# Kernel tuning notes

Hardware: AMD Instinct MI355X
Metric: run time of the kernel (lower is better)

## Reference

```python
import jax, jax.numpy as jnp
import numpy as np
from jax.scipy.stats import norm

K = 2               # select_experts
NOISE_EPS = 0.01
LOSS_COEF = 0.01
CV_EPS = 1e-10


def setup_inputs() -> dict:
    key = jax.random.key(0)
    ks = jax.random.split(key, 8)
    N, D, H, E = 8192, 1024, 4096, 8
    s_in = 1.0 / np.sqrt(D)
    s_h = 1.0 / np.sqrt(H)
    return {
        "x": jax.random.normal(ks[0], (N, D), jnp.float32),
        "noise": jax.random.normal(ks[1], (N, E), jnp.float32),
        "w_gate": jax.random.normal(ks[2], (D, E), jnp.float32) * s_in,
        "w_noise": jax.random.normal(ks[3], (D, E), jnp.float32) * s_in,
        "W1": jax.random.normal(ks[4], (E, D, H), jnp.float32) * s_in,
        "b1": jnp.zeros((E, H), jnp.float32),
        "W2": jax.random.normal(ks[5], (E, H, D), jnp.float32) * s_h,
        "b2": jnp.zeros((E, D), jnp.float32),
    }


def _cv_squared(v):
    # torch .var() is unbiased (ddof=1)
    return v.var(ddof=1) / (v.mean() ** 2 + CV_EPS)


def reference(x, noise, w_gate, w_noise, W1, b1, W2, b2):
    N = x.shape[0]
    # --- noisy top-k gating (training path) ---
    clean_logits = x @ w_gate                                  # [N, E]
    noise_stddev = jax.nn.softplus(x @ w_noise) + NOISE_EPS    # [N, E]
    noisy_logits = clean_logits + noise * noise_stddev         # [N, E]
    top_vals, top_idx = jax.lax.top_k(noisy_logits, K + 1)     # [N, K+1]
    top_k_gates = jax.nn.softmax(top_vals[:, :K], axis=1)      # [N, K]
    gates = jnp.zeros_like(noisy_logits).at[
        jnp.arange(N)[:, None], top_idx[:, :K]
    ].set(top_k_gates)                                         # [N, E]

    # --- load (prob of being in top-k under the gating noise) ---
    thr_in = top_vals[:, K:K + 1]                              # [N, 1]
    thr_out = top_vals[:, K - 1:K]                             # [N, 1]
    is_in = noisy_logits > thr_in
    prob_in = norm.cdf((clean_logits - thr_in) / noise_stddev)
    prob_out = norm.cdf((clean_logits - thr_out) / noise_stddev)
    load = jnp.where(is_in, prob_in, prob_out).sum(0)          # [E]

    importance = gates.sum(0)                                  # [E]
    loss = (_cv_squared(importance) + _cv_squared(load)) * LOSS_COEF

    # --- dense all-expert stack, masked by sparse gates ---
    h = jax.nn.relu(jnp.einsum('nd,edh->neh', x, W1) + b1)     # [N, E, H]
    out = jnp.einsum('neh,ehd->ned', h, W2) + b2               # [N, E, D]
    y = jnp.einsum('ned,ne->nd', out, gates)                   # [N, D]
    return y, loss
```

## Files before the change

### kernel.cpp

```cpp
#include <hip/hip_runtime.h>

typedef unsigned short u16;
typedef unsigned int u32;
typedef __attribute__((ext_vector_type(4))) float f32x4;
typedef __attribute__((ext_vector_type(8))) short short8;
typedef __attribute__((ext_vector_type(4))) unsigned short u16x4;

#define BARR __builtin_amdgcn_s_barrier()
#define VM4  asm volatile("s_waitcnt vmcnt(4)" ::: "memory")
#define VM0  asm volatile("s_waitcnt vmcnt(0)" ::: "memory")

__device__ __forceinline__ u16 f2b(float f){
  u32 u = __float_as_uint(f);
  u = (u + 0x7FFFu + ((u >> 16) & 1u)) >> 16;
  return (u16)u;
}
__device__ __forceinline__ float b2f(u16 h){ return __uint_as_float(((u32)h) << 16); }

__device__ __forceinline__ void gload16(const void* g, void* l){
  __builtin_amdgcn_global_load_lds((__attribute__((address_space(1))) void*)(g),
                                   (__attribute__((address_space(3))) void*)(l), 16, 0, 0);
}

__global__ __launch_bounds__(256) void transpose_cvt2_kernel(const float* __restrict__ W1,
                                                             const float* __restrict__ W2,
                                                             u16* __restrict__ w1t,
                                                             u16* __restrict__ w2t){
  __shared__ float t[64][65];
  int z = blockIdx.z;
  const float* src; u16* dst; int R, C, c0, r0; size_t eo;
  if (z < 8){
    src = W1; dst = w1t; R = 1024; C = 4096;
    c0 = blockIdx.x * 64; r0 = blockIdx.y * 64;
    eo = (size_t)R * C * z;
  } else {
    src = W2; dst = w2t; R = 4096; C = 1024;
    c0 = blockIdx.y * 64; r0 = blockIdx.x * 64;
    eo = (size_t)R * C * (z - 8);
  }
  int tid = threadIdx.x;
  int lr = tid >> 4, lc4 = (tid & 15) * 4;
  #pragma unroll
  for (int i = 0; i < 4; i++){
    int r = lr + i * 16;
    float4 v = *(const float4*)&src[eo + (size_t)(r0 + r) * C + c0 + lc4];
    t[r][lc4] = v.x; t[r][lc4 + 1] = v.y; t[r][lc4 + 2] = v.z; t[r][lc4 + 3] = v.w;
  }
  __syncthreads();
  #pragma unroll
  for (int i = 0; i < 4; i++){
    int c = lr + i * 16;
    u16x4 o = { f2b(t[lc4][c]), f2b(t[lc4 + 1][c]), f2b(t[lc4 + 2][c]), f2b(t[lc4 + 3][c]) };
    *(u16x4*)&dst[eo + (size_t)(c0 + c) * R + r0 + lc4] = o;
  }
}

__global__ __launch_bounds__(256) void gating_kernel(const float* __restrict__ x,
                                                     const float* __restrict__ nz,
                                                     const float* __restrict__ wg,
                                                     const float* __restrict__ wn,
                                                     int* __restrict__ counts,
                                                     int4* __restrict__ rowinfo,
                                                     float* __restrict__ loadrow,
                                                     u16* __restrict__ xb){
  __shared__ float wpart[16][4][17];
  int tid = threadIdx.x, w = tid >> 6, lane = tid & 63;
  int d0 = w * 256 + lane * 4;
  float4 wgA[4], wgB[4], wnA[4], wnB[4];
  #pragma unroll
  for (int k = 0; k < 4; k++){
    wgA[k] = *(const float4*)&wg[(d0 + k) * 8];
    wgB[k] = *(const float4*)&wg[(d0 + k) * 8 + 4];
    wnA[k] = *(const float4*)&wn[(d0 + k) * 8];
    wnB[k] = *(const float4*)&wn[(d0 + k) * 8 + 4];
  }
  int rbase = blockIdx.x * 16;
  for (int r = 0; r < 16; r++){
    int row = rbase + r;
    float4 xv = *(const float4*)&x[(size_t)row * 1024 + d0];
    u16x4 xo = { f2b(xv.x), f2b(xv.y), f2b(xv.z), f2b(xv.w) };
    *(u16x4*)&xb[(size_t)row * 1024 + d0] = xo;
    float ag[8], an[8];
    #pragma unroll
    for (int e = 0; e < 8; e++){ ag[e] = 0.f; an[e] = 0.f; }
    float xk[4] = { xv.x, xv.y, xv.z, xv.w };
    #pragma unroll
    for (int k = 0; k < 4; k++){
      ag[0] = fmaf(xk[k], wgA[k].x, ag[0]); ag[1] = fmaf(xk[k], wgA[k].y, ag[1]);
      ag[2] = fmaf(xk[k], wgA[k].z, ag[2]); ag[3] = fmaf(xk[k], wgA[k].w, ag[3]);
      ag[4] = fmaf(xk[k], wgB[k].x, ag[4]); ag[5] = fmaf(xk[k], wgB[k].y, ag[5]);
      ag[6] = fmaf(xk[k], wgB[k].z, ag[6]); ag[7] = fmaf(xk[k], wgB[k].w, ag[7]);
      an[0] = fmaf(xk[k], wnA[k].x, an[0]); an[1] = fmaf(xk[k], wnA[k].y, an[1]);
      an[2] = fmaf(xk[k], wnA[k].z, an[2]); an[3] = fmaf(xk[k], wnA[k].w, an[3]);
      an[4] = fmaf(xk[k], wnB[k].x, an[4]); an[5] = fmaf(xk[k], wnB[k].y, an[5]);
      an[6] = fmaf(xk[k], wnB[k].z, an[6]); an[7] = fmaf(xk[k], wnB[k].w, an[7]);
    }
    #pragma unroll
    for (int off = 32; off >= 1; off >>= 1){
      #pragma unroll
      for (int e = 0; e < 8; e++){
        ag[e] += __shfl_xor(ag[e], off, 64);
        an[e] += __shfl_xor(an[e], off, 64);
      }
    }
    if (lane == 0){
      #pragma unroll
      for (int e = 0; e < 8; e++){
        wpart[r][w][e] = ag[e];
        wpart[r][w][8 + e] = an[e];
      }
    }
  }
  __syncthreads();
  if (tid < 16){
    int r = tid, row = rbase + r;
    float cg[16];
    #pragma unroll
    for (int v = 0; v < 16; v++)
      cg[v] = wpart[r][0][v] + wpart[r][1][v] + wpart[r][2][v] + wpart[r][3][v];
    float clean[8], sd[8], noisy[8];
    #pragma unroll
    for (int e = 0; e < 8; e++){
      clean[e] = cg[e];
      float v = cg[8 + e];
      float sp = fmaxf(v, 0.f) + log1pf(expf(-fabsf(v)));
      sd[e] = sp + 0.01f;
      noisy[e] = clean[e] + nz[row * 8 + e] * sd[e];
    }
    int i0 = 0, i1 = -1;
    float b0 = -3.4e38f, b1v = -3.4e38f, b2v = -3.4e38f;
    #pragma unroll
    for (int j = 0; j < 8; j++){
      float t = noisy[j];
      if (t > b0){ b2v = b1v; b1v = b0; i1 = i0; b0 = t; i0 = j; }
      else if (t > b1v){ b2v = b1v; b1v = t; i1 = j; }
      else if (t > b2v){ b2v = t; }
    }
    float eg = expf(b1v - b0);
    float g0 = 1.f / (1.f + eg), g1 = eg / (1.f + eg);
    rowinfo[row] = make_int4(i0, i1, __float_as_int(g0), __float_as_int(g1));
    atomicAdd(&counts[i0], 1);
    atomicAdd(&counts[i1], 1);
    float thr_in = b2v, thr_out = b1v;
    #pragma unroll
    for (int e = 0; e < 8; e++){
      bool isin = noisy[e] > thr_in;
      float thr = isin ? thr_in : thr_out;
      float z = (clean[e] - thr) / sd[e];
      loadrow[row * 8 + e] = 0.5f * (1.f + erff(z * 0.70710678118654752f));
    }
  }
}

__global__ __launch_bounds__(256) void fill_kernel(const int* __restrict__ counts,
                                                   const int4* __restrict__ rowinfo,
                                                   int* __restrict__ offs,
                                                   int* __restrict__ cnt2,
                                                   int* __restrict__ tok,
                                                   int* __restrict__ slot_of,
                                                   int* __restrict__ btab){
  __shared__ int loff[8];
  if (threadIdx.x == 0){
    int s = 0;
    for (int e = 0; e < 8; e++){ loff[e] = s; s += counts[e]; }
    if (blockIdx.x == 0){
      int nb = 0;
      for (int e = 0; e < 8; e++){
        offs[e] = loff[e];
        int nbe = (counts[e] + 255) >> 8;
        for (int t = 0; t < nbe; t++) btab[nb++] = (e << 16) | t;
      }
      offs[15] = nb;
    }
  }
  __syncthreads();
  int r = blockIdx.x * 256 + threadIdx.x;
  int4 ri = rowinfo[r];
  int p0 = atomicAdd(&cnt2[ri.x], 1);
  int s0 = loff[ri.x] + p0;
  tok[s0] = r; slot_of[2 * r] = s0;
  int p1 = atomicAdd(&cnt2[ri.y], 1);
  int s1 = loff[ri.y] + p1;
  tok[s1] = r; slot_of[2 * r + 1] = s1;
}

template<int KDIM, bool GATHER, bool RELU, bool PSPLIT>
__global__ __launch_bounds__(512, 1) void ffn8_kernel(
    const u16* __restrict__ Ag, const u16* __restrict__ Bt,
    const float* __restrict__ bias, u16* __restrict__ outp,
    const int* __restrict__ counts, const int* __restrict__ offs,
    const int* __restrict__ btab, const int* __restrict__ tok,
    int nc, int klen, int ostr, size_t pstride)
{
  __shared__ u16 As[2][2][128 * 64];
  __shared__ u16 Bs[2][2][128 * 64];

  int gx = gridDim.x;
  int lin = blockIdx.y * gx + blockIdx.x;
  int total = gx * gridDim.y, chunk = total >> 3;
  int swz = (lin & 7) * chunk + (lin >> 3);
  int bx = swz % gx, tq = swz / gx;
  int nblk = offs[15];
  if (bx >= nblk) return;
  int kh = tq / nc;
  int tn = tq - kh * nc;
  int kbase = kh * klen;
  int niter = klen >> 7;
  int et = btab[bx]; int e = et >> 16, tm = et & 0xffff;
  int cnt = counts[e], off_e = offs[e];

  int tid = threadIdx.x, lane = tid & 63;
  int wid = tid >> 6, wm = wid >> 2, wn = wid & 3;

  int rl0 = tid >> 3, c8 = tid & 7;
  const char* Abase = (const char*)Ag + (size_t)kbase * 2;
  const char* Bbase = (const char*)(Bt + (size_t)e * 4194304) + (size_t)kbase * 2;
  u32 aoff[4], boff[4];
  #pragma unroll
  for (int h = 0; h < 2; h++)
    #pragma unroll
    for (int r = 0; r < 2; r++){
      int rl = h * 128 + r * 64 + rl0;
      int c8s = c8 ^ (rl & 7);
      int rr = tm * 256 + rl;
      int rc = (rr < cnt) ? rr : (cnt - 1);
      size_t arow = GATHER ? (size_t)tok[off_e + rc] : (size_t)(off_e + rc);
      aoff[h * 2 + r] = (u32)(arow * (KDIM * 2) + c8s * 16);
      boff[h * 2 + r] = (u32)((size_t)(tn * 256 + rl) * (KDIM * 2) + c8s * 16);
    }
  int ldst = (tid & ~63) * 8;

  auto stA = [&](int b, int h, int t){
    const char* s = Abase + (size_t)t * 128;
    gload16(s + aoff[h * 2 + 0], &As[b][h][ldst]);
    gload16(s + aoff[h * 2 + 1], &As[b][h][4096 + ldst]);
  };
  auto stB = [&](int b, int h, int t){
    const char* s = Bbase + (size_t)t * 128;
    gload16(s + boff[h * 2 + 0], &Bs[b][h][ldst]);
    gload16(s + boff[h * 2 + 1], &Bs[b][h][4096 + ldst]);
  };

  int lm = lane & 15, lkb = (lane >> 4) * 8;
  short8 Ar[4][2], Br[2][2][2];
  auto ldA = [&](int b, int rh){
    #pragma unroll
    for (int ii = 0; ii < 4; ii++){
      int rl = rh * 64 + ii * 16 + lm;
      #pragma unroll
      for (int ks = 0; ks < 2; ks++){
        int idx = (rl * 64 + ks * 32 + lkb) ^ ((rl & 7) << 3);
        Ar[ii][ks] = *(const short8*)&As[b][wm][idx];
      }
    }
  };
  auto ldB = [&](int b, int ch){
    #pragma unroll
    for (int jj = 0; jj < 2; jj++){
      int rb = wn * 64 + ch * 32 + jj * 16 + lm;
      int hB = rb >> 7, rl = rb & 127;
      #pragma unroll
      for (int ks = 0; ks < 2; ks++){
        int idx = (rl * 64 + ks * 32 + lkb) ^ ((rl & 7) << 3);
        Br[ch][jj][ks] = *(const short8*)&Bs[b][hB][idx];
      }
    }
  };

  f32x4 acc[8][4];
  #pragma unroll
  for (int i = 0; i < 8; i++)
    #pragma unroll
    for (int j = 0; j < 4; j++) acc[i][j] = (f32x4){0.f, 0.f, 0.f, 0.f};

  auto mfmaQ = [&](int rh, int ch){
    __builtin_amdgcn_s_setprio(1);
    #pragma unroll
    for (int ks = 0; ks < 2; ks++)
      #pragma unroll
      for (int ii = 0; ii < 4; ii++)
        #pragma unroll
        for (int jj = 0; jj < 2; jj++)
          acc[rh * 4 + ii][ch * 2 + jj] = __builtin_amdgcn_mfma_f32_16x16x32_bf16(
              Ar[ii][ks], Br[ch][jj][ks], acc[rh * 4 + ii][ch * 2 + jj], 0, 0, 0);
    __builtin_amdgcn_s_setprio(0);
  };

  stA(0, 0, 0); stA(0, 1, 0); stB(0, 0, 0); stB(0, 1, 0);
  stB(1, 0, 1); stA(1, 0, 1);
  VM4; BARR;

  for (int j = 0; j < niter - 1; ++j){
    int t1 = 2 * j + 1, t2 = 2 * j + 2, t3 = 2 * j + 3;
    ldA(0, 0); ldB(0, 0);
    stA(1, 1, t1);
    BARR; mfmaQ(0, 0); ldB(0, 1); BARR;
    stB(1, 1, t1);
    BARR; mfmaQ(0, 1); ldA(0, 1); BARR;
    stB(0, 0, t2);
    BARR; mfmaQ(1, 1); BARR;
    stA(0, 0, t2);
    BARR; mfmaQ(1, 0); VM4; BARR;
    ldA(1, 0); ldB(1, 0);
    stA(0, 1, t2);
    BARR; mfmaQ(0, 0); ldB(1, 1); BARR;
    stB(0, 1, t2);
    BARR; mfmaQ(0, 1); ldA(1, 1); BARR;
    stB(1, 0, t3);
    BARR; mfmaQ(1, 1); BARR;
    stA(1, 0, t3);
    BARR; mfmaQ(1, 0); VM4; BARR;
  }

  {
    int t1 = (klen >> 6) - 1;
    ldA(0, 0); ldB(0, 0);
    stA(1, 1, t1);
    BARR; mfmaQ(0, 0); ldB(0, 1); BARR;
    stB(1, 1, t1);
    BARR; mfmaQ(0, 1); ldA(0, 1); BARR;
    BARR; mfmaQ(1, 1); BARR;
    mfmaQ(1, 0); VM0; BARR;
    ldA(1, 0); ldB(1, 0);
    BARR; mfmaQ(0, 0); ldB(1, 1); BARR;
    BARR; mfmaQ(0, 1); ldA(1, 1); BARR;
    BARR; mfmaQ(1, 1); BARR;
    mfmaQ(1, 0);
  }

  int lr = (lane >> 4) * 4;
  u16* po = outp + (PSPLIT ? (size_t)kh * pstride : 0);
  #pragma unroll
  for (int i = 0; i < 8; i++){
    int row_l = wm * 128 + i * 16 + lr;
    #pragma unroll
    for (int jj = 0; jj < 4; jj++){
      int col = tn * 256 + wn * 64 + jj * 16 + lm;
      float bv = PSPLIT ? 0.f : bias[e * ostr + col];
      #pragma unroll
      for (int q = 0; q < 4; q++){
        int r = tm * 256 + row_l + q;
        if (r < cnt){
          float v = acc[i][jj][q] + bv;
          if (RELU) v = fmaxf(v, 0.f);
          po[(size_t)(off_e + r) * ostr + col] = f2b(v);
        }
      }
    }
  }
}

__global__ __launch_bounds__(256) void combine_kernel(const u16* __restrict__ pb,
                                                      const float* __restrict__ b2,
                                                      const int4* __restrict__ rowinfo,
                                                      const int* __restrict__ slot_of,
                                                      float* __restrict__ y){
  const size_t PS = (size_t)16384 * 1024;
  int w = threadIdx.x >> 6, lane = threadIdx.x & 63;
  int row = blockIdx.x * 4 + w;
  int4 ri = rowinfo[row];
  float g0 = __int_as_float(ri.z), g1 = __int_as_float(ri.w);
  int s0 = slot_of[2 * row], s1 = slot_of[2 * row + 1];
  const u16* pa = pb + ((size_t)s0 << 10);
  const u16* pbb = pb + ((size_t)s1 << 10);
  #pragma unroll
  for (int k = 0; k < 4; k++){
    int c4 = k * 256 + lane * 4;
    float4 sum0 = *(const float4*)&b2[(ri.x << 10) + c4];
    float4 sum1 = *(const float4*)&b2[(ri.y << 10) + c4];
    #pragma unroll
    for (int kh = 0; kh < 4; kh++){
      u16x4 a = *(const u16x4*)&pa[kh * PS + c4];
      u16x4 b = *(const u16x4*)&pbb[kh * PS + c4];
      sum0.x += b2f(a.x); sum0.y += b2f(a.y); sum0.z += b2f(a.z); sum0.w += b2f(a.w);
      sum1.x += b2f(b.x); sum1.y += b2f(b.y); sum1.z += b2f(b.z); sum1.w += b2f(b.w);
    }
    float4 o;
    o.x = g0 * sum0.x + g1 * sum1.x;
    o.y = g0 * sum0.y + g1 * sum1.y;
    o.z = g0 * sum0.z + g1 * sum1.z;
    o.w = g0 * sum0.w + g1 * sum1.w;
    *(float4*)&y[(size_t)row * 1024 + c4] = o;
  }
}

__global__ __launch_bounds__(256) void loss1_kernel(const int4* __restrict__ rowinfo,
                                                    const float* __restrict__ loadrow,
                                                    float* __restrict__ partials){
  __shared__ float part[16][256];
  int tid = threadIdx.x;
  int r = blockIdx.x * 256 + tid;
  int4 ri = rowinfo[r];
  float g0 = __int_as_float(ri.z), g1 = __int_as_float(ri.w);
  f32x4 l0 = *(const f32x4*)&loadrow[r * 8];
  f32x4 l1 = *(const f32x4*)&loadrow[r * 8 + 4];
  #pragma unroll
  for (int e = 0; e < 8; e++){
    part[e][tid] = ((ri.x == e) ? g0 : 0.f) + ((ri.y == e) ? g1 : 0.f);
    part[8 + e][tid] = (e < 4) ? l0[e & 3] : l1[e & 3];
  }
  __syncthreads();
  #pragma unroll
  for (int s = 128; s >= 1; s >>= 1){
    if (tid < s){
      #pragma unroll
      for (int e = 0; e < 16; e++) part[e][tid] += part[e][tid + s];
    }
    __syncthreads();
  }
  if (tid < 16) partials[blockIdx.x * 16 + tid] = part[tid][0];
}

__global__ __launch_bounds__(64) void loss2_kernel(const float* __restrict__ partials,
                                                   float* __restrict__ out_loss){
  __shared__ float tot[16];
  int tid = threadIdx.x;
  if (tid < 16){
    float s = 0.f;
    for (int b = 0; b < 32; b++) s += partials[b * 16 + tid];
    tot[tid] = s;
  }
  __syncthreads();
  if (tid == 0){
    float mi = 0.f, ml = 0.f;
    for (int e = 0; e < 8; e++){ mi += tot[e]; ml += tot[8 + e]; }
    mi *= 0.125f; ml *= 0.125f;
    float vi = 0.f, vl = 0.f;
    for (int e = 0; e < 8; e++){
      float di = tot[e] - mi; vi += di * di;
      float dl = tot[8 + e] - ml; vl += dl * dl;
    }
    vi /= 7.f; vl /= 7.f;
    float cvi = vi / (mi * mi + 1e-10f);
    float cvl = vl / (ml * ml + 1e-10f);
    out_loss[0] = 0.01f * (cvi + cvl);
  }
}

extern "C" void kernel_launch(void* const* d_in, const int* in_sizes, int n_in,
                              void* d_out, int out_size, void* d_ws, size_t ws_size,
                              hipStream_t stream){
  const float* x  = (const float*)d_in[0];
  const float* nz = (const float*)d_in[1];
  const float* wg = (const float*)d_in[2];
  const float* wn = (const float*)d_in[3];
  const float* W1 = (const float*)d_in[4];
  const float* b1 = (const float*)d_in[5];
  const float* W2 = (const float*)d_in[6];
  const float* b2 = (const float*)d_in[7];
  float* y = (float*)d_out;
  float* loss = y + (size_t)8192 * 1024;

  char* ws = (char*)d_ws;
  size_t o = 0;
  auto alloc = [&](size_t bytes){ size_t r = o; o += (bytes + 255) & ~(size_t)255; return r; };
  int*  counts  = (int*)(ws + alloc(64));
  int*  cnt2    = (int*)(ws + alloc(64));
  int*  offs    = (int*)(ws + alloc(64));
  int*  btab    = (int*)(ws + alloc(1024));
  int4* rowinfo = (int4*)(ws + alloc((size_t)8192 * 16));
  int*  slot_of = (int*)(ws + alloc((size_t)16384 * 4));
  int*  tok     = (int*)(ws + alloc((size_t)16384 * 4));
  float* loadrow = (float*)(ws + alloc((size_t)8192 * 8 * 4));
  float* partials = (float*)(ws + alloc(32 * 16 * 4));
  u16*  xb      = (u16*)(ws + alloc((size_t)8192 * 1024 * 2));
  u16*  w1t     = (u16*)(ws + alloc((size_t)8 * 1024 * 4096 * 2));
  u16*  w2t     = (u16*)(ws + alloc((size_t)8 * 1024 * 4096 * 2));
  u16*  h_buf   = (u16*)(ws + alloc((size_t)16384 * 4096 * 2));
  u16*  pbuf    = (u16*)(ws + alloc((size_t)4 * 16384 * 1024 * 2));
  if (o > ws_size) return;

  hipMemsetAsync(ws, 0, 768, stream);

  gating_kernel<<<512, 256, 0, stream>>>(x, nz, wg, wn, counts, rowinfo, loadrow, xb);
  transpose_cvt2_kernel<<<dim3(64, 16, 16), 256, 0, stream>>>(W1, W2, w1t, w2t);
  fill_kernel<<<32, 256, 0, stream>>>(counts, rowinfo, offs, cnt2, tok, slot_of, btab);
  ffn8_kernel<1024, true, true, false><<<dim3(72, 16), 512, 0, stream>>>(
      xb, w1t, b1, h_buf, counts, offs, btab, tok, 16, 1024, 4096, 0);
  ffn8_kernel<4096, false, false, true><<<dim3(72, 16), 512, 0, stream>>>(
      h_buf, w2t, nullptr, pbuf, counts, offs, btab, tok, 4, 1024, 1024,
      (size_t)16384 * 1024);
  combine_kernel<<<2048, 256, 0, stream>>>(pbuf, b2, rowinfo, slot_of, y);
  loss1_kernel<<<32, 256, 0, stream>>>(rowinfo, loadrow, partials);
  loss2_kernel<<<1, 64, 0, stream>>>(partials, loss);
}
```

Before: 683.6 us.

## Merge gating with weight transpose, halve FFN2 split-K, fold loss into combine

Gating and the W1/W2 transpose-to-bf16 work now run in a single prep kernel, dispatched by block index, and the first loss reduction stage runs as extra blocks of the combine kernel. The second FFN GEMM now splits K into 2 partitions instead of 4, each covering 2048 of the 4096 reduction elements, so the partial-sum buffer and combine reads are halved. The aim is fewer launches and less partial-sum traffic. The cost is fewer FFN2 blocks (72x8), which may leave some compute units idle.

```diff
diff --git a/kernel.cpp b/kernel.cpp
--- a/kernel.cpp
+++ b/kernel.cpp
@@ -22,49 +22,55 @@
                                    (__attribute__((address_space(3))) void*)(l), 16, 0, 0);
 }
 
-__global__ __launch_bounds__(256) void transpose_cvt2_kernel(const float* __restrict__ W1,
-                                                             const float* __restrict__ W2,
-                                                             u16* __restrict__ w1t,
-                                                             u16* __restrict__ w2t){
-  __shared__ float t[64][65];
-  int z = blockIdx.z;
-  const float* src; u16* dst; int R, C, c0, r0; size_t eo;
-  if (z < 8){
-    src = W1; dst = w1t; R = 1024; C = 4096;
-    c0 = blockIdx.x * 64; r0 = blockIdx.y * 64;
-    eo = (size_t)R * C * z;
-  } else {
-    src = W2; dst = w2t; R = 4096; C = 1024;
-    c0 = blockIdx.y * 64; r0 = blockIdx.x * 64;
-    eo = (size_t)R * C * (z - 8);
-  }
+__global__ __launch_bounds__(256) void prep_kernel(const float* __restrict__ x,
+                                                   const float* __restrict__ nz,
+                                                   const float* __restrict__ wg,
+                                                   const float* __restrict__ wn,
+                                                   const float* __restrict__ W1,
+                                                   const float* __restrict__ W2,
+                                                   int* __restrict__ counts,
+                                                   int4* __restrict__ rowinfo,
+                                                   float* __restrict__ loadrow,
+                                                   u16* __restrict__ xb,
+                                                   u16* __restrict__ w1t,
+                                                   u16* __restrict__ w2t){
+  __shared__ __align__(16) char SM[17408];
+  int b = blockIdx.x;
   int tid = threadIdx.x;
-  int lr = tid >> 4, lc4 = (tid & 15) * 4;
-  #pragma unroll
-  for (int i = 0; i < 4; i++){
-    int r = lr + i * 16;
-    float4 v = *(const float4*)&src[eo + (size_t)(r0 + r) * C + c0 + lc4];
-    t[r][lc4] = v.x; t[r][lc4 + 1] = v.y; t[r][lc4 + 2] = v.z; t[r][lc4 + 3] = v.w;
-  }
-  __syncthreads();
-  #pragma unroll
-  for (int i = 0; i < 4; i++){
-    int c = lr + i * 16;
-    u16x4 o = { f2b(t[lc4][c]), f2b(t[lc4 + 1][c]), f2b(t[lc4 + 2][c]), f2b(t[lc4 + 3][c]) };
-    *(u16x4*)&dst[eo + (size_t)(c0 + c) * R + r0 + lc4] = o;
-  }
-}
-
-__global__ __launch_bounds__(256) void gating_kernel(const float* __restrict__ x,
-                                                     const float* __restrict__ nz,
-                                                     const float* __restrict__ wg,
-                                                     const float* __restrict__ wn,
-                                                     int* __restrict__ counts,
-                                                     int4* __restrict__ rowinfo,
-                                                     float* __restrict__ loadrow,
-                                                     u16* __restrict__ xb){
-  __shared__ float wpart[16][4][17];
-  int tid = threadIdx.x, w = tid >> 6, lane = tid & 63;
+  if (b >= 512){
+    int t = b - 512;
+    const float* src; u16* dst; int R, C, r0, c0; size_t eo;
+    if (t < 8192){
+      src = W1; dst = w1t; R = 1024; C = 4096;
+      int e = t >> 10, rem = t & 1023;
+      c0 = (rem & 63) * 64; r0 = (rem >> 6) * 64;
+      eo = (size_t)R * C * e;
+    } else {
+      t -= 8192;
+      src = W2; dst = w2t; R = 4096; C = 1024;
+      int e = t >> 10, rem = t & 1023;
+      r0 = (rem & 63) * 64; c0 = (rem >> 6) * 64;
+      eo = (size_t)R * C * e;
+    }
+    float (*tt)[65] = (float(*)[65])SM;
+    int lr = tid >> 4, lc4 = (tid & 15) * 4;
+    #pragma unroll
+    for (int i = 0; i < 4; i++){
+      int r = lr + i * 16;
+      float4 v = *(const float4*)&src[eo + (size_t)(r0 + r) * C + c0 + lc4];
+      tt[r][lc4] = v.x; tt[r][lc4 + 1] = v.y; tt[r][lc4 + 2] = v.z; tt[r][lc4 + 3] = v.w;
+    }
+    __syncthreads();
+    #pragma unroll
+    for (int i = 0; i < 4; i++){
+      int c = lr + i * 16;
+      u16x4 o = { f2b(tt[lc4][c]), f2b(tt[lc4 + 1][c]), f2b(tt[lc4 + 2][c]), f2b(tt[lc4 + 3][c]) };
+      *(u16x4*)&dst[eo + (size_t)(c0 + c) * R + r0 + lc4] = o;
+    }
+    return;
+  }
+  float (*wpart)[4][17] = (float(*)[4][17])SM;
+  int w = tid >> 6, lane = tid & 63;
   int d0 = w * 256 + lane * 4;
   float4 wgA[4], wgB[4], wnA[4], wnB[4];
   #pragma unroll
@@ -74,7 +80,7 @@
     wnA[k] = *(const float4*)&wn[(d0 + k) * 8];
     wnB[k] = *(const float4*)&wn[(d0 + k) * 8 + 4];
   }
-  int rbase = blockIdx.x * 16;
+  int rbase = b * 16;
   for (int r = 0; r < 16; r++){
     int row = rbase + r;
     float4 xv = *(const float4*)&x[(size_t)row * 1024 + d0];
@@ -354,7 +360,34 @@
                                                       const float* __restrict__ b2,
                                                       const int4* __restrict__ rowinfo,
                                                       const int* __restrict__ slot_of,
-                                                      float* __restrict__ y){
+                                                      const float* __restrict__ loadrow,
+                                                      float* __restrict__ y,
+                                                      float* __restrict__ partials){
+  if (blockIdx.x >= 2048){
+    __shared__ float part[16][256];
+    int tid = threadIdx.x;
+    int r = (blockIdx.x - 2048) * 256 + tid;
+    int4 ri = rowinfo[r];
+    float g0 = __int_as_float(ri.z), g1 = __int_as_float(ri.w);
+    f32x4 l0 = *(const f32x4*)&loadrow[r * 8];
+    f32x4 l1 = *(const f32x4*)&loadrow[r * 8 + 4];
+    #pragma unroll
+    for (int e = 0; e < 8; e++){
+      part[e][tid] = ((ri.x == e) ? g0 : 0.f) + ((ri.y == e) ? g1 : 0.f);
+      part[8 + e][tid] = (e < 4) ? l0[e & 3] : l1[e & 3];
+    }
+    __syncthreads();
+    #pragma unroll
+    for (int s = 128; s >= 1; s >>= 1){
+      if (tid < s){
+        #pragma unroll
+        for (int e = 0; e < 16; e++) part[e][tid] += part[e][tid + s];
+      }
+      __syncthreads();
+    }
+    if (tid < 16) partials[(blockIdx.x - 2048) * 16 + tid] = part[tid][0];
+    return;
+  }
   const size_t PS = (size_t)16384 * 1024;
   int w = threadIdx.x >> 6, lane = threadIdx.x & 63;
   int row = blockIdx.x * 4 + w;
@@ -369,7 +402,7 @@
     float4 sum0 = *(const float4*)&b2[(ri.x << 10) + c4];
     float4 sum1 = *(const float4*)&b2[(ri.y << 10) + c4];
     #pragma unroll
-    for (int kh = 0; kh < 4; kh++){
+    for (int kh = 0; kh < 2; kh++){
       u16x4 a = *(const u16x4*)&pa[kh * PS + c4];
       u16x4 b = *(const u16x4*)&pbb[kh * PS + c4];
       sum0.x += b2f(a.x); sum0.y += b2f(a.y); sum0.z += b2f(a.z); sum0.w += b2f(a.w);
@@ -382,33 +415,6 @@
     o.w = g0 * sum0.w + g1 * sum1.w;
     *(float4*)&y[(size_t)row * 1024 + c4] = o;
   }
-}
-
-__global__ __launch_bounds__(256) void loss1_kernel(const int4* __restrict__ rowinfo,
-                                                    const float* __restrict__ loadrow,
-                                                    float* __restrict__ partials){
-  __shared__ float part[16][256];
-  int tid = threadIdx.x;
-  int r = blockIdx.x * 256 + tid;
-  int4 ri = rowinfo[r];
-  float g0 = __int_as_float(ri.z), g1 = __int_as_float(ri.w);
-  f32x4 l0 = *(const f32x4*)&loadrow[r * 8];
-  f32x4 l1 = *(const f32x4*)&loadrow[r * 8 + 4];
-  #pragma unroll
-  for (int e = 0; e < 8; e++){
-    part[e][tid] = ((ri.x == e) ? g0 : 0.f) + ((ri.y == e) ? g1 : 0.f);
-    part[8 + e][tid] = (e < 4) ? l0[e & 3] : l1[e & 3];
-  }
-  __syncthreads();
-  #pragma unroll
-  for (int s = 128; s >= 1; s >>= 1){
-    if (tid < s){
-      #pragma unroll
-      for (int e = 0; e < 16; e++) part[e][tid] += part[e][tid + s];
-    }
-    __syncthreads();
-  }
-  if (tid < 16) partials[blockIdx.x * 16 + tid] = part[tid][0];
 }
 
 __global__ __launch_bounds__(64) void loss2_kernel(const float* __restrict__ partials,
@@ -467,20 +473,19 @@
   u16*  w1t     = (u16*)(ws + alloc((size_t)8 * 1024 * 4096 * 2));
   u16*  w2t     = (u16*)(ws + alloc((size_t)8 * 1024 * 4096 * 2));
   u16*  h_buf   = (u16*)(ws + alloc((size_t)16384 * 4096 * 2));
-  u16*  pbuf    = (u16*)(ws + alloc((size_t)4 * 16384 * 1024 * 2));
+  u16*  pbuf    = (u16*)(ws + alloc((size_t)2 * 16384 * 1024 * 2));
   if (o > ws_size) return;
 
   hipMemsetAsync(ws, 0, 768, stream);
 
-  gating_kernel<<<512, 256, 0, stream>>>(x, nz, wg, wn, counts, rowinfo, loadrow, xb);
-  transpose_cvt2_kernel<<<dim3(64, 16, 16), 256, 0, stream>>>(W1, W2, w1t, w2t);
+  prep_kernel<<<16896, 256, 0, stream>>>(x, nz, wg, wn, W1, W2,
+                                         counts, rowinfo, loadrow, xb, w1t, w2t);
   fill_kernel<<<32, 256, 0, stream>>>(counts, rowinfo, offs, cnt2, tok, slot_of, btab);
   ffn8_kernel<1024, true, true, false><<<dim3(72, 16), 512, 0, stream>>>(
       xb, w1t, b1, h_buf, counts, offs, btab, tok, 16, 1024, 4096, 0);
-  ffn8_kernel<4096, false, false, true><<<dim3(72, 16), 512, 0, stream>>>(
-      h_buf, w2t, nullptr, pbuf, counts, offs, btab, tok, 4, 1024, 1024,
+  ffn8_kernel<4096, false, false, true><<<dim3(72, 8), 512, 0, stream>>>(
+      h_buf, w2t, nullptr, pbuf, counts, offs, btab, tok, 4, 2048, 1024,
       (size_t)16384 * 1024);
-  combine_kernel<<<2048, 256, 0, stream>>>(pbuf, b2, rowinfo, slot_of, y);
-  loss1_kernel<<<32, 256, 0, stream>>>(rowinfo, loadrow, partials);
+  combine_kernel<<<2080, 256, 0, stream>>>(pbuf, b2, rowinfo, slot_of, loadrow, y, partials);
   loss2_kernel<<<1, 64, 0, stream>>>(partials, loss);
 }
```

Measured after the change: 632.2 us. 1.08x faster.
